# Kernel tuning notes

Hardware: AMD Instinct MI355X
Metric: run time of the kernel (lower is better)

## Reference

```python
import jax, jax.numpy as jnp
import numpy as np

N_NODES = 50000
N_EDGES = 800000
D = 128  # node_dim == edge_dim
NEG_SLOPE = 0.2


def setup_inputs() -> dict:
    key = jax.random.key(0)
    ks = jax.random.split(key, 16)
    w = lambda k, shp: (jax.random.normal(k, shp, dtype=jnp.float32) * 0.02)
    b = lambda: jnp.zeros((D,), dtype=jnp.float32)
    return {
        "V": jax.random.normal(ks[0], (N_NODES, D), dtype=jnp.float32),
        "E": jax.random.normal(ks[1], (N_EDGES, D), dtype=jnp.float32),
        "src": jax.random.randint(ks[2], (N_EDGES,), 0, N_NODES, dtype=jnp.int32),
        "dst": jax.random.randint(ks[3], (N_EDGES,), 0, N_NODES, dtype=jnp.int32),
        # NodePooling: two node_dim->node_dim linears
        "Wp1": w(ks[4], (D, D)), "bp1": b(),
        "Wp2": w(ks[5], (D, D)), "bp2": b(),
        # GenMessage.A: MLP with nb_mlp_layer=2 linears (edge_dim->edge_dim)
        "WA1": w(ks[6], (D, D)), "bA1": b(),
        "WA2": w(ks[7], (D, D)), "bA2": b(),
        # GenMessage.B (scale) and .C (shift): edge_dim->node_dim
        "WB": w(ks[8], (D, D)), "bB": b(),
        "WC": w(ks[9], (D, D)), "bC": b(),
    }


def reference(V, E, src, dst, Wp1, bp1, Wp2, bp2, WA1, bA1, WA2, bA2, WB, bB, WC, bC):
    lrelu = lambda x: jax.nn.leaky_relu(x, NEG_SLOPE)
    # V = act(V); G.ndata['V'] = pooling(V)
    Vp = lrelu(lrelu(V) @ Wp1.T + bp1) @ Wp2.T + bp2  # [N, D]
    # edge MLP on edge features (ReLU between linears, none after last)
    x = jax.nn.relu(E @ WA1.T + bA1) @ WA2.T + bA2    # [E, D]
    scale = jax.nn.sigmoid(x @ WB.T + bB)             # [E, D]
    shift = x @ WC.T + bC                             # [E, D]
    # per-edge gated message using gathered source node features
    msg = scale * Vp[src] + shift                     # [E, D]
    # scatter-sum into destination nodes (dgl.fn.sum)
    out = jax.ops.segment_sum(msg, dst, num_segments=N_NODES)  # [N, D]
    return out
```

## Files before the change

### kernel.cpp

```cpp
#include <hip/hip_runtime.h>
#include <hip/hip_bf16.h>

typedef __attribute__((ext_vector_type(8))) short bf16x8;
typedef __attribute__((ext_vector_type(4))) float f32x4;

#define DD 128

static __device__ __forceinline__ unsigned short f2bf(float f) {
    __bf16 h = (__bf16)f;
    return __builtin_bit_cast(unsigned short, h);
}
static __device__ __forceinline__ unsigned int pk2bf(float lo, float hi) {
    return ((unsigned int)f2bf(hi) << 16) | (unsigned int)f2bf(lo);
}
static __device__ __forceinline__ float bf2f(unsigned short h) {
    unsigned int u = ((unsigned int)h) << 16;
    return __builtin_bit_cast(float, u);
}

static __device__ __forceinline__ void lds_barrier() {
    asm volatile("s_waitcnt lgkmcnt(0)" ::: "memory");
    __builtin_amdgcn_s_barrier();
    asm volatile("" ::: "memory");
}
static __device__ __forceinline__ void lds_fence() {
    asm volatile("s_waitcnt lgkmcnt(0)" ::: "memory");
}

__global__ __launch_bounds__(256) void k_convert_hist(
    const float* __restrict__ w0, const float* __restrict__ w1,
    const float* __restrict__ w2, const float* __restrict__ w3,
    const float* __restrict__ w4, const float* __restrict__ w5,
    unsigned short* __restrict__ wbf,
    const int* __restrict__ dst, int* __restrict__ counts, int nE, int use_perm) {
    int i = blockIdx.x * blockDim.x + threadIdx.x;
    if (i < 6 * 16384) {
        int m = i >> 14, k = i & 16383;
        const float* s = (m == 0) ? w0 : (m == 1) ? w1 : (m == 2) ? w2 : (m == 3) ? w3
                         : (m == 4) ? w4 : w5;
        wbf[i] = f2bf(s[k]);
    }
    if (use_perm)
        for (int e = i; e < nE; e += gridDim.x * blockDim.x)
            atomicAdd(&counts[dst[e]], 1);
}

__global__ __launch_bounds__(256) void k_scanA(const int* __restrict__ counts,
                                               int* __restrict__ cursor,
                                               int* __restrict__ partials, int nN) {
    __shared__ int ps[256];
    const int tid = threadIdx.x;
    const int i = blockIdx.x * 256 + tid;
    int v = (i < nN) ? counts[i] : 0;
    ps[tid] = v;
    __syncthreads();
    for (int off = 1; off < 256; off <<= 1) {
        int add = (tid >= off) ? ps[tid - off] : 0;
        __syncthreads();
        ps[tid] += add;
        __syncthreads();
    }
    if (i < nN) cursor[i] = ps[tid] - v;
    if (tid == 255) partials[blockIdx.x] = ps[255];
}

__global__ __launch_bounds__(256) void k_scanB(int* __restrict__ cursor,
                                               const int* __restrict__ partials,
                                               int nN, int nB) {
    __shared__ int ps[256];
    const int tid = threadIdx.x;
    int v = 0;
    for (int j = tid; j < blockIdx.x; j += 256) v += partials[j];
    ps[tid] = v;
    __syncthreads();
    for (int off = 1; off < 256; off <<= 1) {
        int add = (tid >= off) ? ps[tid - off] : 0;
        __syncthreads();
        ps[tid] += add;
        __syncthreads();
    }
    const int offset = ps[255];
    const int i = blockIdx.x * 256 + tid;
    if (i < nN) cursor[i] += offset;
}

__global__ __launch_bounds__(256, 3) void k_nodes(
    const float* __restrict__ V, const unsigned short* __restrict__ wbf,
    const float* __restrict__ bp1, const float* __restrict__ bp2,
    unsigned short* __restrict__ Vp, int nN, int nTiles,
    const int* __restrict__ src, const int* __restrict__ dst,
    int* __restrict__ cursor, int* __restrict__ perm,
    int* __restrict__ srcS, int* __restrict__ dstS, int nE, int use_perm)
{
    if (use_perm)
        for (int e = blockIdx.x * blockDim.x + threadIdx.x; e < nE; e += gridDim.x * blockDim.x) {
            int d = dst[e];
            int pos = atomicAdd(&cursor[d], 1);
            perm[pos] = e;
            srcS[pos] = src[e];
            dstS[pos] = d;
        }

    const int lane = threadIdx.x & 63;
    const int wave = threadIdx.x >> 6;
    const int lr = lane & 15, lg = lane >> 4;

    bf16x8 B1[2][4], B2[2][4];
#pragma unroll
    for (int ct = 0; ct < 2; ++ct)
#pragma unroll
        for (int kk = 0; kk < 4; ++kk) {
            int j = wave * 32 + ct * 16 + lr;
            int k0 = kk * 32 + lg * 8;
            B1[ct][kk] = *(const bf16x8*)(wbf + 0 * 16384 + j * DD + k0);
            B2[ct][kk] = *(const bf16x8*)(wbf + 1 * 16384 + j * DD + k0);
        }
    float b1v[2], b2v[2];
#pragma unroll
    for (int ct = 0; ct < 2; ++ct) {
        int c = wave * 32 + ct * 16 + lr;
        b1v[ct] = bp1[c]; b2v[ct] = bp2[c];
    }
    __shared__ alignas(16) unsigned short xb[32][132];

    for (int t = blockIdx.x; t < nTiles; t += gridDim.x) {
        const int r0 = t * 32;
        bf16x8 A[2][4];
#pragma unroll
        for (int rg = 0; rg < 2; ++rg)
#pragma unroll
            for (int kk = 0; kk < 4; ++kk) {
                int row = r0 + rg * 16 + lr; if (row >= nN) row = nN - 1;
                const float4* p = (const float4*)(V + (size_t)row * DD + kk * 32 + lg * 8);
                float4 f0 = p[0], f1 = p[1];
                float v[8] = {f0.x, f0.y, f0.z, f0.w, f1.x, f1.y, f1.z, f1.w};
                bf16x8 a;
#pragma unroll
                for (int e = 0; e < 8; ++e) {
                    float x = v[e];
                    x = x > 0.f ? x : 0.2f * x;
                    a[e] = (short)f2bf(x);
                }
                A[rg][kk] = a;
            }
#pragma unroll
        for (int rg = 0; rg < 2; ++rg)
#pragma unroll
            for (int ct = 0; ct < 2; ++ct) {
                f32x4 acc = {0.f, 0.f, 0.f, 0.f};
#pragma unroll
                for (int kk = 0; kk < 4; ++kk)
                    acc = __builtin_amdgcn_mfma_f32_16x16x32_bf16(A[rg][kk], B1[ct][kk], acc, 0, 0, 0);
#pragma unroll
                for (int r = 0; r < 4; ++r) {
                    float x = acc[r] + b1v[ct];
                    x = x > 0.f ? x : 0.2f * x;
                    xb[rg * 16 + lg * 4 + r][wave * 32 + ct * 16 + lr] = f2bf(x);
                }
            }
        lds_barrier();
        bf16x8 A2[2][4];
#pragma unroll
        for (int rg = 0; rg < 2; ++rg)
#pragma unroll
            for (int kk = 0; kk < 4; ++kk)
                A2[rg][kk] = *(const bf16x8*)&xb[rg * 16 + lr][kk * 32 + lg * 8];
#pragma unroll
        for (int rg = 0; rg < 2; ++rg)
#pragma unroll
            for (int ct = 0; ct < 2; ++ct) {
                f32x4 acc = {0.f, 0.f, 0.f, 0.f};
#pragma unroll
                for (int kk = 0; kk < 4; ++kk)
                    acc = __builtin_amdgcn_mfma_f32_16x16x32_bf16(A2[rg][kk], B2[ct][kk], acc, 0, 0, 0);
#pragma unroll
                for (int r = 0; r < 4; ++r) {
                    int row = r0 + rg * 16 + lg * 4 + r;
                    if (row < nN)
                        Vp[(size_t)row * DD + wave * 32 + ct * 16 + lr] = f2bf(acc[r] + b2v[ct]);
                }
            }
        lds_barrier();
    }
}

__global__ __launch_bounds__(256, 2) void k_edges(
    const float* __restrict__ E, const int* __restrict__ src, const int* __restrict__ dst,
    const int* __restrict__ perm, const int* __restrict__ srcS, const int* __restrict__ dstS,
    int use_perm,
    const unsigned short* __restrict__ wbf,
    const float* __restrict__ bA1, const float* __restrict__ bA2,
    const float* __restrict__ bB, const float* __restrict__ bC,
    const unsigned short* __restrict__ Vp, float* __restrict__ out, int nE, int nTiles)
{
    const int lane = threadIdx.x & 63;
    const int wave = threadIdx.x >> 6;
    const int lr = lane & 15, lg = lane >> 4;
    const int srow = threadIdx.x >> 3;
    const int schunk = threadIdx.x & 7;

    bf16x8 B1[2][4], B2[2][4], B3[2][4], B4[2][4];
#pragma unroll
    for (int ct = 0; ct < 2; ++ct)
#pragma unroll
        for (int kk = 0; kk < 4; ++kk) {
            int j = wave * 32 + ct * 16 + lr;
            int k0 = kk * 32 + lg * 8;
            const unsigned short* p = wbf + 2 * 16384 + j * DD + k0;
            B1[ct][kk] = *(const bf16x8*)(p);
            B2[ct][kk] = *(const bf16x8*)(p + 16384);
            B3[ct][kk] = *(const bf16x8*)(p + 32768);
            B4[ct][kk] = *(const bf16x8*)(p + 49152);
        }
    float b1v[2], b2v[2], b3v[2], b4v[2];
#pragma unroll
    for (int ct = 0; ct < 2; ++ct) {
        int c = wave * 32 + ct * 16 + lr;
        b1v[ct] = bA1[c]; b2v[ct] = bA2[c]; b3v[ct] = bB[c]; b4v[ct] = bC[c];
    }
    __shared__ alignas(16) unsigned short xb[2][32][132];
    __shared__ alignas(16) unsigned short Eb[2][32][132];
    __shared__ alignas(8)  unsigned short gv[32][140];
    __shared__ alignas(16) float msgw[4][32][34];
    __shared__ int dstb[32];

    const int gstep = gridDim.x;
    int t = blockIdx.x;

    auto loadMeta = [&](int i, int& pe, int& sl, int& pd) {
        bool valid = (i < nE); if (!valid) i = nE - 1;
        if (use_perm) { pe = perm[i]; sl = srcS[i]; pd = dstS[i]; }
        else          { pe = i;       sl = src[i];  pd = dst[i];  }
        if (!valid) pd = -1;
    };

    int pe_t, sl_t, pd;
    loadMeta(t * 32 + srow, pe_t, sl_t, pd);
    int peN, slN, pdN;
    loadMeta((t + gstep) * 32 + srow, peN, slN, pdN);
    uint2 g0, g1, g2, g3;
    {
        const uint2* vp2 = (const uint2*)(Vp + (size_t)sl_t * DD);
        g0 = vp2[schunk]; g1 = vp2[schunk + 8]; g2 = vp2[schunk + 16]; g3 = vp2[schunk + 24];
    }
    float4 pf0, pf1, pf2, pf3;
    {
        const float4* np = (const float4*)(E + (size_t)peN * DD + schunk * 16);
        pf0 = np[0]; pf1 = np[1]; pf2 = np[2]; pf3 = np[3];
    }
    {
        const float4* p = (const float4*)(E + (size_t)pe_t * DD + schunk * 16);
        float4 f0 = p[0], f1 = p[1], f2 = p[2], f3 = p[3];
        uint4 w0 = make_uint4(pk2bf(f0.x, f0.y), pk2bf(f0.z, f0.w),
                              pk2bf(f1.x, f1.y), pk2bf(f1.z, f1.w));
        uint4 w1 = make_uint4(pk2bf(f2.x, f2.y), pk2bf(f2.z, f2.w),
                              pk2bf(f3.x, f3.y), pk2bf(f3.z, f3.w));
        uint4* wp = (uint4*)&Eb[0][srow][schunk * 16];
        wp[0] = w0; wp[1] = w1;
    }
    lds_barrier();
    int cur = 0;

    for (; t < nTiles; t += gstep) {
        bf16x8 A[2][4];
#pragma unroll
        for (int rg = 0; rg < 2; ++rg)
#pragma unroll
            for (int kk = 0; kk < 4; ++kk)
                A[rg][kk] = *(const bf16x8*)&Eb[cur][rg * 16 + lr][kk * 32 + lg * 8];
#pragma unroll
        for (int rg = 0; rg < 2; ++rg)
#pragma unroll
            for (int ct = 0; ct < 2; ++ct) {
                f32x4 acc = {0.f, 0.f, 0.f, 0.f};
                __builtin_amdgcn_s_setprio(1);
#pragma unroll
                for (int kk = 0; kk < 4; ++kk)
                    acc = __builtin_amdgcn_mfma_f32_16x16x32_bf16(A[rg][kk], B1[ct][kk], acc, 0, 0, 0);
                __builtin_amdgcn_s_setprio(0);
#pragma unroll
                for (int r = 0; r < 4; ++r) {
                    float x = fmaxf(acc[r] + b1v[ct], 0.f);
                    xb[0][rg * 16 + lg * 4 + r][wave * 32 + ct * 16 + lr] = f2bf(x);
                }
            }
        lds_barrier();
        *(uint2*)&gv[srow][schunk * 4]      = g0;
        *(uint2*)&gv[srow][schunk * 4 + 32] = g1;
        *(uint2*)&gv[srow][schunk * 4 + 64] = g2;
        *(uint2*)&gv[srow][schunk * 4 + 96] = g3;
        if (schunk == 0) dstb[srow] = pd;
        {
            uint4 w0 = make_uint4(pk2bf(pf0.x, pf0.y), pk2bf(pf0.z, pf0.w),
                                  pk2bf(pf1.x, pf1.y), pk2bf(pf1.z, pf1.w));
            uint4 w1 = make_uint4(pk2bf(pf2.x, pf2.y), pk2bf(pf2.z, pf2.w),
                                  pk2bf(pf3.x, pf3.y), pk2bf(pf3.z, pf3.w));
            uint4* wp = (uint4*)&Eb[cur ^ 1][srow][schunk * 16];
            wp[0] = w0; wp[1] = w1;
        }
        int pe2, sl2, pd2;
        loadMeta((t + 2 * gstep) * 32 + srow, pe2, sl2, pd2);
        float4 nf0, nf1, nf2, nf3;
        {
            const float4* np = (const float4*)(E + (size_t)pe2 * DD + schunk * 16);
            nf0 = np[0]; nf1 = np[1]; nf2 = np[2]; nf3 = np[3];
        }
        {
            const uint2* nvp2 = (const uint2*)(Vp + (size_t)slN * DD);
            g0 = nvp2[schunk]; g1 = nvp2[schunk + 8]; g2 = nvp2[schunk + 16]; g3 = nvp2[schunk + 24];
        }
        bf16x8 A2[2][4];
#pragma unroll
        for (int rg = 0; rg < 2; ++rg)
#pragma unroll
            for (int kk = 0; kk < 4; ++kk)
                A2[rg][kk] = *(const bf16x8*)&xb[0][rg * 16 + lr][kk * 32 + lg * 8];
#pragma unroll
        for (int rg = 0; rg < 2; ++rg)
#pragma unroll
            for (int ct = 0; ct < 2; ++ct) {
                f32x4 acc = {0.f, 0.f, 0.f, 0.f};
                __builtin_amdgcn_s_setprio(1);
#pragma unroll
                for (int kk = 0; kk < 4; ++kk)
                    acc = __builtin_amdgcn_mfma_f32_16x16x32_bf16(A2[rg][kk], B2[ct][kk], acc, 0, 0, 0);
                __builtin_amdgcn_s_setprio(0);
#pragma unroll
                for (int r = 0; r < 4; ++r)
                    xb[1][rg * 16 + lg * 4 + r][wave * 32 + ct * 16 + lr] = f2bf(acc[r] + b2v[ct]);
            }
        lds_barrier();
        bf16x8 A3[2][4];
#pragma unroll
        for (int rg = 0; rg < 2; ++rg)
#pragma unroll
            for (int kk = 0; kk < 4; ++kk)
                A3[rg][kk] = *(const bf16x8*)&xb[1][rg * 16 + lr][kk * 32 + lg * 8];
#pragma unroll
        for (int rg = 0; rg < 2; ++rg)
#pragma unroll
            for (int ct = 0; ct < 2; ++ct) {
                f32x4 aB = {0.f, 0.f, 0.f, 0.f}, aC = {0.f, 0.f, 0.f, 0.f};
                __builtin_amdgcn_s_setprio(1);
#pragma unroll
                for (int kk = 0; kk < 4; ++kk) {
                    aB = __builtin_amdgcn_mfma_f32_16x16x32_bf16(A3[rg][kk], B3[ct][kk], aB, 0, 0, 0);
                    aC = __builtin_amdgcn_mfma_f32_16x16x32_bf16(A3[rg][kk], B4[ct][kk], aC, 0, 0, 0);
                }
                __builtin_amdgcn_s_setprio(0);
#pragma unroll
                for (int r = 0; r < 4; ++r) {
                    float e = __expf(-(aB[r] + b3v[ct]));
                    float sc = __builtin_amdgcn_rcpf(1.f + e);
                    float sh = aC[r] + b4v[ct];
                    float v = bf2f(gv[rg * 16 + lg * 4 + r][wave * 32 + ct * 16 + lr]);
                    msgw[wave][rg * 16 + lg * 4 + r][ct * 16 + lr] = sc * v + sh;
                }
            }
        lds_fence();
        {
            const int cw = lane & 31;
            const int half = lane >> 5;
            const int col = wave * 32 + cw;
            const int rbase = half * 16;
            float acc = 0.f;
#pragma unroll
            for (int rr = 0; rr < 16; ++rr) {
                const int rrow = rbase + rr;
                acc += msgw[wave][rrow][cw];
                int d = dstb[rrow];
                bool flush = (rr == 15) || (dstb[rrow + 1] != d);
                if (flush) {
                    if (d >= 0)
                        unsafeAtomicAdd(out + (size_t)d * DD + col, acc);
                    acc = 0.f;
                }
            }
        }
        cur ^= 1;
        pf0 = nf0; pf1 = nf1; pf2 = nf2; pf3 = nf3;
        pd = pdN; pdN = pd2; slN = sl2;
    }
}

extern "C" void kernel_launch(void* const* d_in, const int* in_sizes, int n_in,
                              void* d_out, int out_size, void* d_ws, size_t ws_size,
                              hipStream_t stream) {
    const float* V   = (const float*)d_in[0];
    const float* E   = (const float*)d_in[1];
    const int*   src = (const int*)d_in[2];
    const int*   dst = (const int*)d_in[3];
    const float* Wp1 = (const float*)d_in[4];  const float* bp1 = (const float*)d_in[5];
    const float* Wp2 = (const float*)d_in[6];  const float* bp2 = (const float*)d_in[7];
    const float* WA1 = (const float*)d_in[8];  const float* bA1 = (const float*)d_in[9];
    const float* WA2 = (const float*)d_in[10]; const float* bA2 = (const float*)d_in[11];
    const float* WB  = (const float*)d_in[12]; const float* bB  = (const float*)d_in[13];
    const float* WC  = (const float*)d_in[14]; const float* bC  = (const float*)d_in[15];
    float* out = (float*)d_out;

    const int nN = in_sizes[0] / DD;
    const int nE = in_sizes[1] / DD;
    const int nTilesN = (nN + 31) / 32;
    const int nTilesE = (nE + 31) / 32;
    const int nB = (nN + 255) / 256;

    char* wsb = (char*)d_ws;
    unsigned short* wbf = (unsigned short*)wsb;
    unsigned short* Vp  = (unsigned short*)(wsb + 196608);
    size_t off = 196608 + (size_t)nN * 256;
    int* counts   = (int*)(wsb + off); off += (size_t)nN * 4;
    int* cursor   = (int*)(wsb + off); off += (size_t)nN * 4;
    int* perm     = (int*)(wsb + off); off += (size_t)nE * 4;
    int* srcS     = (int*)(wsb + off); off += (size_t)nE * 4;
    int* dstS     = (int*)(wsb + off); off += (size_t)nE * 4;
    int* partials = (int*)(wsb + off); off += (size_t)nB * 4;
    int use_perm = (ws_size >= off) ? 1 : 0;

    hipMemsetAsync(d_out, 0, (size_t)out_size * sizeof(float), stream);
    if (use_perm) hipMemsetAsync(counts, 0, (size_t)nN * 4, stream);

    k_convert_hist<<<1024, 256, 0, stream>>>(Wp1, Wp2, WA1, WA2, WB, WC, wbf,
                                             dst, counts, nE, use_perm);
    if (use_perm) {
        k_scanA<<<nB, 256, 0, stream>>>(counts, cursor, partials, nN);
        k_scanB<<<nB, 256, 0, stream>>>(cursor, partials, nN, nB);
    }

    int gN = nTilesN < 768 ? nTilesN : 768;
    k_nodes<<<gN, 256, 0, stream>>>(V, wbf, bp1, bp2, Vp, nN, nTilesN,
                                    src, dst, cursor, perm, srcS, dstS, nE, use_perm);
    int gE = nTilesE < 512 ? nTilesE : 512;
    k_edges<<<gE, 256, 0, stream>>>(E, src, dst, perm, srcS, dstS, use_perm, wbf,
                                    bA1, bA2, bB, bC, Vp, out, nE, nTilesE);
}
```

Before: 340.1 us.

## Restructure edge kernel to single-wave blocks streaming weights from cache

The edge kernel moves from 256-thread blocks, where each of four waves owns 32 output columns with weights held in registers, to 64-thread single-wave blocks that compute all 128 columns per 32-edge tile. Weight fragments are now reloaded from global/L2 for each column tile instead of staying resident. E rows go straight into registers, are converted to bf16 there, and are prefetched one tile ahead, replacing the LDS double buffer. The aim is to remove block-wide barriers and raise occupancy, with the grid growing to 2048 blocks. The cost is repeated weight-load traffic and more serialized MFMA work per wave.

```diff
diff --git a/kernel.cpp b/kernel.cpp
--- a/kernel.cpp
+++ b/kernel.cpp
@@ -9,9 +9,6 @@
 static __device__ __forceinline__ unsigned short f2bf(float f) {
     __bf16 h = (__bf16)f;
     return __builtin_bit_cast(unsigned short, h);
-}
-static __device__ __forceinline__ unsigned int pk2bf(float lo, float hi) {
-    return ((unsigned int)f2bf(hi) << 16) | (unsigned int)f2bf(lo);
 }
 static __device__ __forceinline__ float bf2f(unsigned short h) {
     unsigned int u = ((unsigned int)h) << 16;
@@ -184,7 +181,7 @@
     }
 }
 
-__global__ __launch_bounds__(256, 2) void k_edges(
+__global__ __launch_bounds__(64) void k_edges(
     const float* __restrict__ E, const int* __restrict__ src, const int* __restrict__ dst,
     const int* __restrict__ perm, const int* __restrict__ srcS, const int* __restrict__ dstS,
     int use_perm,
@@ -193,193 +190,185 @@
     const float* __restrict__ bB, const float* __restrict__ bC,
     const unsigned short* __restrict__ Vp, float* __restrict__ out, int nE, int nTiles)
 {
-    const int lane = threadIdx.x & 63;
-    const int wave = threadIdx.x >> 6;
+    const int lane = threadIdx.x;
     const int lr = lane & 15, lg = lane >> 4;
-    const int srow = threadIdx.x >> 3;
-    const int schunk = threadIdx.x & 7;
-
-    bf16x8 B1[2][4], B2[2][4], B3[2][4], B4[2][4];
-#pragma unroll
-    for (int ct = 0; ct < 2; ++ct)
-#pragma unroll
-        for (int kk = 0; kk < 4; ++kk) {
-            int j = wave * 32 + ct * 16 + lr;
-            int k0 = kk * 32 + lg * 8;
-            const unsigned short* p = wbf + 2 * 16384 + j * DD + k0;
-            B1[ct][kk] = *(const bf16x8*)(p);
-            B2[ct][kk] = *(const bf16x8*)(p + 16384);
-            B3[ct][kk] = *(const bf16x8*)(p + 32768);
-            B4[ct][kk] = *(const bf16x8*)(p + 49152);
-        }
-    float b1v[2], b2v[2], b3v[2], b4v[2];
-#pragma unroll
-    for (int ct = 0; ct < 2; ++ct) {
-        int c = wave * 32 + ct * 16 + lr;
-        b1v[ct] = bA1[c]; b2v[ct] = bA2[c]; b3v[ct] = bB[c]; b4v[ct] = bC[c];
-    }
-    __shared__ alignas(16) unsigned short xb[2][32][132];
-    __shared__ alignas(16) unsigned short Eb[2][32][132];
-    __shared__ alignas(8)  unsigned short gv[32][140];
-    __shared__ alignas(16) float msgw[4][32][34];
+
+    __shared__ alignas(16) unsigned short xb[32][132];
+    __shared__ alignas(16) float msgs[32][17];
     __shared__ int dstb[32];
 
     const int gstep = gridDim.x;
     int t = blockIdx.x;
 
-    auto loadMeta = [&](int i, int& pe, int& sl, int& pd) {
-        bool valid = (i < nE); if (!valid) i = nE - 1;
-        if (use_perm) { pe = perm[i]; sl = srcS[i]; pd = dstS[i]; }
-        else          { pe = i;       sl = src[i];  pd = dst[i];  }
-        if (!valid) pd = -1;
+    auto edgeId = [&](int i) -> int {
+        if (i >= nE) i = nE - 1;
+        return use_perm ? perm[i] : i;
     };
-
-    int pe_t, sl_t, pd;
-    loadMeta(t * 32 + srow, pe_t, sl_t, pd);
-    int peN, slN, pdN;
-    loadMeta((t + gstep) * 32 + srow, peN, slN, pdN);
-    uint2 g0, g1, g2, g3;
+    auto srcAt = [&](int i) -> int {
+        if (i >= nE) i = nE - 1;
+        return use_perm ? srcS[i] : src[i];
+    };
+    auto dstAt = [&](int i) -> int {
+        if (i >= nE) return -1;
+        return use_perm ? dstS[i] : dst[i];
+    };
+
+    int pe0 = edgeId(t * 32 + lr);
+    int pe1 = edgeId(t * 32 + 16 + lr);
+    int slc = srcAt(t * 32 + (lane >> 1));
+    int pdc = dstAt(t * 32 + lane);
+    float4 raw[2][4][2];
+#pragma unroll
+    for (int rg = 0; rg < 2; ++rg)
+#pragma unroll
+        for (int kk = 0; kk < 4; ++kk) {
+            const float4* p = (const float4*)(E + (size_t)(rg ? pe1 : pe0) * DD + kk * 32 + lg * 8);
+            raw[rg][kk][0] = p[0]; raw[rg][kk][1] = p[1];
+        }
+    uint2 gr[16];
     {
-        const uint2* vp2 = (const uint2*)(Vp + (size_t)sl_t * DD);
-        g0 = vp2[schunk]; g1 = vp2[schunk + 8]; g2 = vp2[schunk + 16]; g3 = vp2[schunk + 24];
-    }
-    float4 pf0, pf1, pf2, pf3;
-    {
-        const float4* np = (const float4*)(E + (size_t)peN * DD + schunk * 16);
-        pf0 = np[0]; pf1 = np[1]; pf2 = np[2]; pf3 = np[3];
-    }
-    {
-        const float4* p = (const float4*)(E + (size_t)pe_t * DD + schunk * 16);
-        float4 f0 = p[0], f1 = p[1], f2 = p[2], f3 = p[3];
-        uint4 w0 = make_uint4(pk2bf(f0.x, f0.y), pk2bf(f0.z, f0.w),
-                              pk2bf(f1.x, f1.y), pk2bf(f1.z, f1.w));
-        uint4 w1 = make_uint4(pk2bf(f2.x, f2.y), pk2bf(f2.z, f2.w),
-                              pk2bf(f3.x, f3.y), pk2bf(f3.z, f3.w));
-        uint4* wp = (uint4*)&Eb[0][srow][schunk * 16];
-        wp[0] = w0; wp[1] = w1;
-    }
-    lds_barrier();
-    int cur = 0;
+        const uint2* vp2 = (const uint2*)(Vp + (size_t)slc * DD) + (lane & 1) * 16;
+#pragma unroll
+        for (int c = 0; c < 16; ++c) gr[c] = vp2[c];
+    }
 
     for (; t < nTiles; t += gstep) {
         bf16x8 A[2][4];
 #pragma unroll
         for (int rg = 0; rg < 2; ++rg)
 #pragma unroll
+            for (int kk = 0; kk < 4; ++kk) {
+                float4 f0 = raw[rg][kk][0], f1 = raw[rg][kk][1];
+                bf16x8 a;
+                a[0] = (short)f2bf(f0.x); a[1] = (short)f2bf(f0.y);
+                a[2] = (short)f2bf(f0.z); a[3] = (short)f2bf(f0.w);
+                a[4] = (short)f2bf(f1.x); a[5] = (short)f2bf(f1.y);
+                a[6] = (short)f2bf(f1.z); a[7] = (short)f2bf(f1.w);
+                A[rg][kk] = a;
+            }
+        if (lane < 32) dstb[lane] = pdc;
+#pragma unroll
+        for (int ct = 0; ct < 8; ++ct) {
+            const unsigned short* wB = wbf + 2 * 16384 + (ct * 16 + lr) * DD + lg * 8;
+            bf16x8 Bt[4];
+#pragma unroll
+            for (int kk = 0; kk < 4; ++kk) Bt[kk] = *(const bf16x8*)(wB + kk * 32);
+            float bv = bA1[ct * 16 + lr];
+#pragma unroll
+            for (int rg = 0; rg < 2; ++rg) {
+                f32x4 acc = {0.f, 0.f, 0.f, 0.f};
+#pragma unroll
+                for (int kk = 0; kk < 4; ++kk)
+                    acc = __builtin_amdgcn_mfma_f32_16x16x32_bf16(A[rg][kk], Bt[kk], acc, 0, 0, 0);
+#pragma unroll
+                for (int r = 0; r < 4; ++r)
+                    xb[rg * 16 + lg * 4 + r][ct * 16 + lr] = f2bf(fmaxf(acc[r] + bv, 0.f));
+            }
+        }
+        lds_fence();
+        bf16x8 A2[2][4];
+#pragma unroll
+        for (int rg = 0; rg < 2; ++rg)
+#pragma unroll
             for (int kk = 0; kk < 4; ++kk)
-                A[rg][kk] = *(const bf16x8*)&Eb[cur][rg * 16 + lr][kk * 32 + lg * 8];
-#pragma unroll
-        for (int rg = 0; rg < 2; ++rg)
-#pragma unroll
-            for (int ct = 0; ct < 2; ++ct) {
+                A2[rg][kk] = *(const bf16x8*)&xb[rg * 16 + lr][kk * 32 + lg * 8];
+        lds_fence();
+#pragma unroll
+        for (int ct = 0; ct < 8; ++ct) {
+            const unsigned short* wB = wbf + 3 * 16384 + (ct * 16 + lr) * DD + lg * 8;
+            bf16x8 Bt[4];
+#pragma unroll
+            for (int kk = 0; kk < 4; ++kk) Bt[kk] = *(const bf16x8*)(wB + kk * 32);
+            float bv = bA2[ct * 16 + lr];
+#pragma unroll
+            for (int rg = 0; rg < 2; ++rg) {
                 f32x4 acc = {0.f, 0.f, 0.f, 0.f};
-                __builtin_amdgcn_s_setprio(1);
 #pragma unroll
                 for (int kk = 0; kk < 4; ++kk)
-                    acc = __builtin_amdgcn_mfma_f32_16x16x32_bf16(A[rg][kk], B1[ct][kk], acc, 0, 0, 0);
-                __builtin_amdgcn_s_setprio(0);
-#pragma unroll
-                for (int r = 0; r < 4; ++r) {
-                    float x = fmaxf(acc[r] + b1v[ct], 0.f);
-                    xb[0][rg * 16 + lg * 4 + r][wave * 32 + ct * 16 + lr] = f2bf(x);
-                }
-            }
-        lds_barrier();
-        *(uint2*)&gv[srow][schunk * 4]      = g0;
-        *(uint2*)&gv[srow][schunk * 4 + 32] = g1;
-        *(uint2*)&gv[srow][schunk * 4 + 64] = g2;
-        *(uint2*)&gv[srow][schunk * 4 + 96] = g3;
-        if (schunk == 0) dstb[srow] = pd;
-        {
-            uint4 w0 = make_uint4(pk2bf(pf0.x, pf0.y), pk2bf(pf0.z, pf0.w),
-                                  pk2bf(pf1.x, pf1.y), pk2bf(pf1.z, pf1.w));
-            uint4 w1 = make_uint4(pk2bf(pf2.x, pf2.y), pk2bf(pf2.z, pf2.w),
-                                  pk2bf(pf3.x, pf3.y), pk2bf(pf3.z, pf3.w));
-            uint4* wp = (uint4*)&Eb[cur ^ 1][srow][schunk * 16];
-            wp[0] = w0; wp[1] = w1;
-        }
-        int pe2, sl2, pd2;
-        loadMeta((t + 2 * gstep) * 32 + srow, pe2, sl2, pd2);
-        float4 nf0, nf1, nf2, nf3;
-        {
-            const float4* np = (const float4*)(E + (size_t)pe2 * DD + schunk * 16);
-            nf0 = np[0]; nf1 = np[1]; nf2 = np[2]; nf3 = np[3];
-        }
-        {
-            const uint2* nvp2 = (const uint2*)(Vp + (size_t)slN * DD);
-            g0 = nvp2[schunk]; g1 = nvp2[schunk + 8]; g2 = nvp2[schunk + 16]; g3 = nvp2[schunk + 24];
-        }
-        bf16x8 A2[2][4];
+                    acc = __builtin_amdgcn_mfma_f32_16x16x32_bf16(A2[rg][kk], Bt[kk], acc, 0, 0, 0);
+#pragma unroll
+                for (int r = 0; r < 4; ++r)
+                    xb[rg * 16 + lg * 4 + r][ct * 16 + lr] = f2bf(acc[r] + bv);
+            }
+        }
+        lds_fence();
+        bf16x8 A3[2][4];
 #pragma unroll
         for (int rg = 0; rg < 2; ++rg)
 #pragma unroll
             for (int kk = 0; kk < 4; ++kk)
-                A2[rg][kk] = *(const bf16x8*)&xb[0][rg * 16 + lr][kk * 32 + lg * 8];
-#pragma unroll
-        for (int rg = 0; rg < 2; ++rg)
-#pragma unroll
-            for (int ct = 0; ct < 2; ++ct) {
-                f32x4 acc = {0.f, 0.f, 0.f, 0.f};
-                __builtin_amdgcn_s_setprio(1);
-#pragma unroll
-                for (int kk = 0; kk < 4; ++kk)
-                    acc = __builtin_amdgcn_mfma_f32_16x16x32_bf16(A2[rg][kk], B2[ct][kk], acc, 0, 0, 0);
-                __builtin_amdgcn_s_setprio(0);
-#pragma unroll
-                for (int r = 0; r < 4; ++r)
-                    xb[1][rg * 16 + lg * 4 + r][wave * 32 + ct * 16 + lr] = f2bf(acc[r] + b2v[ct]);
-            }
-        lds_barrier();
-        bf16x8 A3[2][4];
-#pragma unroll
-        for (int rg = 0; rg < 2; ++rg)
-#pragma unroll
-            for (int kk = 0; kk < 4; ++kk)
-                A3[rg][kk] = *(const bf16x8*)&xb[1][rg * 16 + lr][kk * 32 + lg * 8];
-#pragma unroll
-        for (int rg = 0; rg < 2; ++rg)
-#pragma unroll
-            for (int ct = 0; ct < 2; ++ct) {
-                f32x4 aB = {0.f, 0.f, 0.f, 0.f}, aC = {0.f, 0.f, 0.f, 0.f};
-                __builtin_amdgcn_s_setprio(1);
-#pragma unroll
-                for (int kk = 0; kk < 4; ++kk) {
-                    aB = __builtin_amdgcn_mfma_f32_16x16x32_bf16(A3[rg][kk], B3[ct][kk], aB, 0, 0, 0);
-                    aC = __builtin_amdgcn_mfma_f32_16x16x32_bf16(A3[rg][kk], B4[ct][kk], aC, 0, 0, 0);
-                }
-                __builtin_amdgcn_s_setprio(0);
-#pragma unroll
-                for (int r = 0; r < 4; ++r) {
-                    float e = __expf(-(aB[r] + b3v[ct]));
-                    float sc = __builtin_amdgcn_rcpf(1.f + e);
-                    float sh = aC[r] + b4v[ct];
-                    float v = bf2f(gv[rg * 16 + lg * 4 + r][wave * 32 + ct * 16 + lr]);
-                    msgw[wave][rg * 16 + lg * 4 + r][ct * 16 + lr] = sc * v + sh;
-                }
-            }
+                A3[rg][kk] = *(const bf16x8*)&xb[rg * 16 + lr][kk * 32 + lg * 8];
         lds_fence();
         {
-            const int cw = lane & 31;
-            const int half = lane >> 5;
-            const int col = wave * 32 + cw;
-            const int rbase = half * 16;
-            float acc = 0.f;
-#pragma unroll
-            for (int rr = 0; rr < 16; ++rr) {
-                const int rrow = rbase + rr;
-                acc += msgw[wave][rrow][cw];
-                int d = dstb[rrow];
-                bool flush = (rr == 15) || (dstb[rrow + 1] != d);
-                if (flush) {
-                    if (d >= 0)
-                        unsafeAtomicAdd(out + (size_t)d * DD + col, acc);
-                    acc = 0.f;
-                }
-            }
-        }
-        cur ^= 1;
-        pf0 = nf0; pf1 = nf1; pf2 = nf2; pf3 = nf3;
-        pd = pdN; pdN = pd2; slN = sl2;
+            const int grow = lane >> 1, ghalf = lane & 1;
+#pragma unroll
+            for (int c = 0; c < 16; ++c)
+                *(uint2*)&xb[grow][ghalf * 64 + c * 4] = gr[c];
+        }
+        int pe0n = edgeId((t + gstep) * 32 + lr);
+        int pe1n = edgeId((t + gstep) * 32 + 16 + lr);
+        int sln  = srcAt((t + gstep) * 32 + (lane >> 1));
+        int pdn  = dstAt((t + gstep) * 32 + lane);
+#pragma unroll
+        for (int rg = 0; rg < 2; ++rg)
+#pragma unroll
+            for (int kk = 0; kk < 4; ++kk) {
+                const float4* p = (const float4*)(E + (size_t)(rg ? pe1n : pe0n) * DD + kk * 32 + lg * 8);
+                raw[rg][kk][0] = p[0]; raw[rg][kk][1] = p[1];
+            }
+        lds_fence();
+#pragma unroll
+        for (int ct = 0; ct < 8; ++ct) {
+            const unsigned short* wB3 = wbf + 4 * 16384 + (ct * 16 + lr) * DD + lg * 8;
+            const unsigned short* wB4 = wbf + 5 * 16384 + (ct * 16 + lr) * DD + lg * 8;
+            bf16x8 B3t[4], B4t[4];
+#pragma unroll
+            for (int kk = 0; kk < 4; ++kk) {
+                B3t[kk] = *(const bf16x8*)(wB3 + kk * 32);
+                B4t[kk] = *(const bf16x8*)(wB4 + kk * 32);
+            }
+            float b3 = bB[ct * 16 + lr], b4 = bC[ct * 16 + lr];
+#pragma unroll
+            for (int rg = 0; rg < 2; ++rg) {
+                f32x4 aB = {0.f, 0.f, 0.f, 0.f}, aC = {0.f, 0.f, 0.f, 0.f};
+#pragma unroll
+                for (int kk = 0; kk < 4; ++kk) {
+                    aB = __builtin_amdgcn_mfma_f32_16x16x32_bf16(A3[rg][kk], B3t[kk], aB, 0, 0, 0);
+                    aC = __builtin_amdgcn_mfma_f32_16x16x32_bf16(A3[rg][kk], B4t[kk], aC, 0, 0, 0);
+                }
+#pragma unroll
+                for (int r = 0; r < 4; ++r) {
+                    float e = __expf(-(aB[r] + b3));
+                    float sc = __builtin_amdgcn_rcpf(1.f + e);
+                    float sh = aC[r] + b4;
+                    float v = bf2f(xb[rg * 16 + lg * 4 + r][ct * 16 + lr]);
+                    msgs[rg * 16 + lg * 4 + r][lr] = sc * v + sh;
+                }
+            }
+            lds_fence();
+            if (lane < 32) {
+                const int col = lane & 15, half = lane >> 4;
+                float acc = 0.f;
+#pragma unroll
+                for (int rr = 0; rr < 16; ++rr) {
+                    const int row = half * 16 + rr;
+                    acc += msgs[row][col];
+                    int d = dstb[row];
+                    bool flush = (rr == 15) || (dstb[row + 1] != d);
+                    if (flush) {
+                        if (d >= 0)
+                            unsafeAtomicAdd(out + (size_t)d * DD + ct * 16 + col, acc);
+                        acc = 0.f;
+                    }
+                }
+            }
+        }
+        {
+            const uint2* vp2 = (const uint2*)(Vp + (size_t)sln * DD) + (lane & 1) * 16;
+#pragma unroll
+            for (int c = 0; c < 16; ++c) gr[c] = vp2[c];
+        }
+        pdc = pdn; slc = sln;
     }
 }
 
@@ -429,7 +418,7 @@
     int gN = nTilesN < 768 ? nTilesN : 768;
     k_nodes<<<gN, 256, 0, stream>>>(V, wbf, bp1, bp2, Vp, nN, nTilesN,
                                     src, dst, cursor, perm, srcS, dstS, nE, use_perm);
-    int gE = nTilesE < 512 ? nTilesE : 512;
-    k_edges<<<gE, 256, 0, stream>>>(E, src, dst, perm, srcS, dstS, use_perm, wbf,
-                                    bA1, bA2, bB, bC, Vp, out, nE, nTilesE);
-}
+    int gE = nTilesE < 2048 ? nTilesE : 2048;
+    k_edges<<<gE, 64, 0, stream>>>(E, src, dst, perm, srcS, dstS, use_perm, wbf,
+                                   bA1, bA2, bB, bC, Vp, out, nE, nTilesE);
+}
```

Measured after the change: 803.4 us. 2.36x slower.
